# Performance work log

Measured on AMD Instinct MI355X. Metric: run time of the kernel, lower is better.

## Reference

```python
import jax, jax.numpy as jnp
import numpy as np

N_NODES = 8192
N_EDGES = 262144
N_PATHS = 1000000
MAX_PATH = 5
EDGE_DIM = 32


def setup_inputs() -> dict:
    key = jax.random.key(0)
    k1, k2, k3, k4, k5, k6, k7 = jax.random.split(key, 7)
    return {
        "x": jax.random.normal(k1, (N_NODES, EDGE_DIM), dtype=jnp.float32),
        "edge_attr": jax.random.normal(k2, (N_EDGES, EDGE_DIM), dtype=jnp.float32),
        "edge_weights": jax.random.normal(k3, (MAX_PATH, EDGE_DIM), dtype=jnp.float32),
        "paths": jax.random.randint(k4, (N_PATHS, MAX_PATH), 0, N_EDGES, dtype=jnp.int64),
        "path_lens": jax.random.randint(k5, (N_PATHS,), 0, MAX_PATH + 1, dtype=jnp.int64),
        "src": jax.random.randint(k6, (N_PATHS,), 0, N_NODES, dtype=jnp.int64),
        "dst": jax.random.randint(k7, (N_PATHS,), 0, N_NODES, dtype=jnp.int64),
    }


def reference(x, edge_attr, edge_weights, paths, path_lens, src, dst):
    # Per-path gather of edge features: [P, L, D]
    feats = edge_attr[paths]
    # Per-hop dot product with the learned per-hop weight vector: [P, L]
    hop_dots = jnp.einsum("pld,ld->pl", feats, edge_weights)
    # Mask hops beyond each path's length (original slices path[:len]).
    L = edge_weights.shape[0]
    hop_mask = jnp.arange(L)[None, :] < path_lens[:, None]  # [P, L]
    s = jnp.sum(jnp.where(hop_mask, hop_dots, 0.0), axis=1)  # [P]
    lens_f = path_lens.astype(s.dtype)
    # Mean over path hops (zero-length paths -> 0, matching nan_to_num).
    enc = jnp.where(path_lens > 0, s / jnp.maximum(lens_f, 1.0), 0.0)
    n = x.shape[0]
    cij = jnp.zeros((n, n), dtype=x.dtype).at[src, dst].set(enc)
    return jnp.nan_to_num(cij)
```

## Files before the change

kernel.cpp:

```cpp
#include <hip/hip_runtime.h>

#define N_NODES_C 8192
#define MAX_PATH_C 5
#define EDGE_DIM_C 32

typedef unsigned int uint4_v __attribute__((ext_vector_type(4)));

#define WS_CNT    0
#define WS_OFFS   8192
#define WS_CURSOR 24576
#define WS_PATHID 32768
#define WS_ENC    (32768 + 1048576)

__global__ void __launch_bounds__(256) k_init(unsigned int* __restrict__ cnt)
{
    int i = blockIdx.x * blockDim.x + threadIdx.x;
    if (i < N_NODES_C) cnt[i] = 0u;
}

__global__ void __launch_bounds__(256) k_hist_enc(
    const float* __restrict__ edge_attr,
    const float* __restrict__ edge_weights,
    const int* __restrict__ paths,
    const int* __restrict__ path_lens,
    const int* __restrict__ src,
    unsigned int* __restrict__ cnt,
    float* __restrict__ enc_out, int P)
{
    __shared__ __align__(16) float w[MAX_PATH_C * EDGE_DIM_C];
    for (int i = threadIdx.x; i < MAX_PATH_C * EDGE_DIM_C; i += blockDim.x)
        w[i] = edge_weights[i];
    __syncthreads();

    int p = blockIdx.x * blockDim.x + threadIdx.x;
    if (p >= P) return;

    atomicAdd(&cnt[src[p]], 1u);

    int len = path_lens[p];
    float s = 0.0f;
    #pragma unroll
    for (int l = 0; l < MAX_PATH_C; ++l) {
        if (l < len) {
            long long e = (long long)paths[p * MAX_PATH_C + l];
            const float4* __restrict__ row =
                (const float4*)(edge_attr + e * EDGE_DIM_C);
            const float4* wr = (const float4*)(w + l * EDGE_DIM_C);
            float acc = 0.0f;
            #pragma unroll
            for (int j = 0; j < EDGE_DIM_C / 4; ++j) {
                float4 a = row[j];
                float4 b = wr[j];
                acc += a.x * b.x + a.y * b.y + a.z * b.z + a.w * b.w;
            }
            s += acc;
        }
    }
    float enc = (len > 0) ? s / (float)len : 0.0f;
    if (isnan(enc)) enc = 0.0f;
    enc_out[p] = enc;
}

__global__ void __launch_bounds__(1024) k_scan(
    const unsigned int* __restrict__ cnt,
    unsigned int* __restrict__ offs,
    unsigned int* __restrict__ cursor)
{
    __shared__ unsigned int part[1024];
    int t = threadIdx.x;
    unsigned int local[8];
    unsigned int mysum = 0;
    #pragma unroll
    for (int j = 0; j < 8; ++j) { local[j] = cnt[t * 8 + j]; mysum += local[j]; }
    part[t] = mysum;
    __syncthreads();
    for (int off = 1; off < 1024; off <<= 1) {
        unsigned int v = 0;
        if (t >= off) v = part[t - off];
        __syncthreads();
        if (t >= off) part[t] += v;
        __syncthreads();
    }
    unsigned int run = part[t] - mysum;
    #pragma unroll
    for (int j = 0; j < 8; ++j) {
        offs[t * 8 + j] = run;
        cursor[t * 8 + j] = run;
        run += local[j];
    }
    if (t == 1023) offs[N_NODES_C] = run;
}

__global__ void __launch_bounds__(256) k_scatter(
    const int* __restrict__ src,
    unsigned int* __restrict__ cursor,
    unsigned int* __restrict__ pathid, int P)
{
    int p = blockIdx.x * blockDim.x + threadIdx.x;
    if (p >= P) return;
    unsigned int pos = atomicAdd(&cursor[src[p]], 1u);
    pathid[pos] = (unsigned int)p;
}

__global__ void __launch_bounds__(256) k_sweep(
    const unsigned int* __restrict__ offs,
    const unsigned int* __restrict__ pathid,
    const float* __restrict__ enc,
    const int* __restrict__ dst,
    float* __restrict__ out)
{
    __shared__ __align__(16) unsigned int row[N_NODES_C];
    const int r = blockIdx.x;
    const int t = threadIdx.x;

    uint4_v* row4 = (uint4_v*)row;
    uint4_v z = (uint4_v)(0u);
    #pragma unroll
    for (int j = 0; j < 8; ++j) row4[j * 256 + t] = z;
    __syncthreads();

    const unsigned int beg = offs[r], end = offs[r + 1];
    for (unsigned int i = beg + t; i < end; i += 256) {
        unsigned int p = pathid[i];
        atomicMax(&row[dst[p]], p + 1u);
    }
    __syncthreads();
    for (unsigned int i = beg + t; i < end; i += 256) {
        unsigned int p = pathid[i];
        int d = dst[p];
        if (row[d] == p + 1u) row[d] = __float_as_uint(enc[p]);
    }
    __syncthreads();

    uint4_v* out4 = (uint4_v*)(out + (size_t)r * N_NODES_C);
    #pragma unroll
    for (int j = 0; j < 8; ++j)
        __builtin_nontemporal_store(row4[j * 256 + t], &out4[j * 256 + t]);
}

extern "C" void kernel_launch(void* const* d_in, const int* in_sizes, int n_in,
                              void* d_out, int out_size, void* d_ws, size_t ws_size,
                              hipStream_t stream)
{
    const float* edge_attr    = (const float*)d_in[1];
    const float* edge_weights = (const float*)d_in[2];
    const int*   paths        = (const int*)d_in[3];
    const int*   path_lens    = (const int*)d_in[4];
    const int*   src          = (const int*)d_in[5];
    const int*   dst          = (const int*)d_in[6];
    float* out = (float*)d_out;
    const int P = in_sizes[4];

    unsigned int* ws_u = (unsigned int*)d_ws;
    unsigned int* cnt    = ws_u + WS_CNT;
    unsigned int* offs   = ws_u + WS_OFFS;
    unsigned int* cursor = ws_u + WS_CURSOR;
    unsigned int* pathid = ws_u + WS_PATHID;
    float*        enc    = (float*)(ws_u + WS_ENC);

    const int threads = 256;
    const int pblocks = (P + threads - 1) / threads;

    k_init<<<(N_NODES_C + threads - 1) / threads, threads, 0, stream>>>(cnt);
    k_hist_enc<<<pblocks, threads, 0, stream>>>(
        edge_attr, edge_weights, paths, path_lens, src, cnt, enc, P);
    k_scan<<<1, 1024, 0, stream>>>(cnt, offs, cursor);
    k_scatter<<<pblocks, threads, 0, stream>>>(src, cursor, pathid, P);
    k_sweep<<<N_NODES_C, threads, 0, stream>>>(offs, pathid, enc, dst, out);
}
```

Before: 174.6 us.

## Precompute per-edge hop dot products before per-path gather

Adds a kernel that computes, once per edge, its dot product with each of the five per-hop weight vectors and stores them in a padded 8-float table. Each path then gathers one float per hop instead of a 128-byte edge row plus a 32-element dot product. The histogram-counter zeroing moves into the new kernel, so one launch is dropped. The cost is an extra full pass over edge_attr and an 8 MB workspace table, in exchange for far less random gather traffic across a million paths.

```diff
diff --git a/kernel.cpp b/kernel.cpp
--- a/kernel.cpp
+++ b/kernel.cpp
@@ -1,6 +1,7 @@
 #include <hip/hip_runtime.h>
 
 #define N_NODES_C 8192
+#define N_EDGES_C 262144
 #define MAX_PATH_C 5
 #define EDGE_DIM_C 32
 
@@ -11,27 +12,53 @@
 #define WS_CURSOR 24576
 #define WS_PATHID 32768
 #define WS_ENC    (32768 + 1048576)
+#define WS_D      (WS_ENC + 1048576)
 
-__global__ void __launch_bounds__(256) k_init(unsigned int* __restrict__ cnt)
+__global__ void __launch_bounds__(256) k_edge_dots(
+    const float* __restrict__ edge_attr,
+    const float* __restrict__ edge_weights,
+    float* __restrict__ D,
+    unsigned int* __restrict__ cnt)
 {
-    int i = blockIdx.x * blockDim.x + threadIdx.x;
-    if (i < N_NODES_C) cnt[i] = 0u;
+    __shared__ __align__(16) float w[MAX_PATH_C * EDGE_DIM_C];
+    for (int i = threadIdx.x; i < MAX_PATH_C * EDGE_DIM_C; i += blockDim.x)
+        w[i] = edge_weights[i];
+    __syncthreads();
+
+    int e = blockIdx.x * blockDim.x + threadIdx.x;
+    if (e < N_NODES_C) cnt[e] = 0u;
+    if (e >= N_EDGES_C) return;
+
+    const float4* __restrict__ row = (const float4*)(edge_attr + (size_t)e * EDGE_DIM_C);
+    float4 a[EDGE_DIM_C / 4];
+    #pragma unroll
+    for (int j = 0; j < EDGE_DIM_C / 4; ++j) a[j] = row[j];
+
+    float d[MAX_PATH_C];
+    #pragma unroll
+    for (int l = 0; l < MAX_PATH_C; ++l) {
+        const float4* wr = (const float4*)(w + l * EDGE_DIM_C);
+        float acc = 0.0f;
+        #pragma unroll
+        for (int j = 0; j < EDGE_DIM_C / 4; ++j) {
+            float4 b = wr[j];
+            acc += a[j].x * b.x + a[j].y * b.y + a[j].z * b.z + a[j].w * b.w;
+        }
+        d[l] = acc;
+    }
+    float4* Dp = (float4*)(D + (size_t)e * 8);
+    Dp[0] = make_float4(d[0], d[1], d[2], d[3]);
+    Dp[1] = make_float4(d[4], 0.0f, 0.0f, 0.0f);
 }
 
-__global__ void __launch_bounds__(256) k_hist_enc(
-    const float* __restrict__ edge_attr,
-    const float* __restrict__ edge_weights,
+__global__ void __launch_bounds__(256) k_path_enc(
+    const float* __restrict__ D,
     const int* __restrict__ paths,
     const int* __restrict__ path_lens,
     const int* __restrict__ src,
     unsigned int* __restrict__ cnt,
     float* __restrict__ enc_out, int P)
 {
-    __shared__ __align__(16) float w[MAX_PATH_C * EDGE_DIM_C];
-    for (int i = threadIdx.x; i < MAX_PATH_C * EDGE_DIM_C; i += blockDim.x)
-        w[i] = edge_weights[i];
-    __syncthreads();
-
     int p = blockIdx.x * blockDim.x + threadIdx.x;
     if (p >= P) return;
 
@@ -42,18 +69,8 @@
     #pragma unroll
     for (int l = 0; l < MAX_PATH_C; ++l) {
         if (l < len) {
-            long long e = (long long)paths[p * MAX_PATH_C + l];
-            const float4* __restrict__ row =
-                (const float4*)(edge_attr + e * EDGE_DIM_C);
-            const float4* wr = (const float4*)(w + l * EDGE_DIM_C);
-            float acc = 0.0f;
-            #pragma unroll
-            for (int j = 0; j < EDGE_DIM_C / 4; ++j) {
-                float4 a = row[j];
-                float4 b = wr[j];
-                acc += a.x * b.x + a.y * b.y + a.z * b.z + a.w * b.w;
-            }
-            s += acc;
+            int e = paths[p * MAX_PATH_C + l];
+            s += D[(size_t)e * 8 + l];
         }
     }
     float enc = (len > 0) ? s / (float)len : 0.0f;
@@ -157,13 +174,15 @@
     unsigned int* cursor = ws_u + WS_CURSOR;
     unsigned int* pathid = ws_u + WS_PATHID;
     float*        enc    = (float*)(ws_u + WS_ENC);
+    float*        D      = (float*)(ws_u + WS_D);
 
     const int threads = 256;
     const int pblocks = (P + threads - 1) / threads;
 
-    k_init<<<(N_NODES_C + threads - 1) / threads, threads, 0, stream>>>(cnt);
-    k_hist_enc<<<pblocks, threads, 0, stream>>>(
-        edge_attr, edge_weights, paths, path_lens, src, cnt, enc, P);
+    k_edge_dots<<<N_EDGES_C / threads, threads, 0, stream>>>(
+        edge_attr, edge_weights, D, cnt);
+    k_path_enc<<<pblocks, threads, 0, stream>>>(
+        D, paths, path_lens, src, cnt, enc, P);
     k_scan<<<1, 1024, 0, stream>>>(cnt, offs, cursor);
     k_scatter<<<pblocks, threads, 0, stream>>>(src, cursor, pathid, P);
     k_sweep<<<N_NODES_C, threads, 0, stream>>>(offs, pathid, enc, dst, out);
```

Result: no change. 174.6 us (+0.0%).
